# Kernel tuning notes

Measured on AMD Instinct MI355X. Metric: run time of the kernel, lower is better.

## Reference

```python
import jax, jax.numpy as jnp
import numpy as np

HEADS = 8
DIM_HEAD = 64
TOP_K = 1024
KMEANS_ITERS = 4  # the original KMeans class is external; we use Lloyd's algorithm, init = first TOP_K points


def chan_ln(x, g, b):
    # ChanLayerNorm3D: normalize over channel dim (axis=1), biased variance
    m = x.mean(axis=1, keepdims=True)
    v = x.var(axis=1, keepdims=True)
    return g.reshape(1, -1, 1, 1, 1) * (x - m) / (jnp.sqrt(v) + 1e-6) + b.reshape(1, -1, 1, 1, 1)


def kmeans_fit(x, k, iters):
    # x: [N, d] -> centroids [k, d]
    cent0 = x[:k]

    def step(_, cent):
        d2 = (x * x).sum(-1, keepdims=True) - 2.0 * (x @ cent.T) + (cent * cent).sum(-1)
        assign = jnp.argmin(d2, axis=-1)
        sums = jax.ops.segment_sum(x, assign, num_segments=k)
        cnt = jax.ops.segment_sum(jnp.ones((x.shape[0],), x.dtype), assign, num_segments=k)
        new = sums / jnp.maximum(cnt, 1.0)[:, None]
        return jnp.where(cnt[:, None] > 0, new, cent)  # keep old centroid for empty clusters

    return jax.lax.fori_loop(0, iters, step, cent0)


def select_best_idx(q, k, top_k):
    # q: [B, i, d], k: [B, j, d] -> indices [B, top_k] of keys farthest (L1) from their assigned q-centroid
    B, j, d = k.shape
    qf = q.reshape(-1, d)
    kf = k.reshape(-1, d)
    cent = kmeans_fit(qf, top_k, KMEANS_ITERS)
    d2 = (kf * kf).sum(-1, keepdims=True) - 2.0 * (kf @ cent.T) + (cent * cent).sum(-1)
    kc = jnp.argmin(d2, axis=-1)  # predict cluster of each key
    centers = cent[kc].reshape(B, j, d)
    dist = jnp.abs(centers - k).sum(-1)  # [B, j], L1 distance to assigned centroid
    return jnp.argsort(-dist, axis=1)[:, :top_k]


def dpca(query_source, context, w_q, w_kv, w_out, cn_g, cn_b, qn_g, qn_b, on_g, on_b, gamma):
    b, c, D, H, W = query_source.shape
    ctx = chan_ln(context, cn_g, cn_b)
    qs = chan_ln(query_source, qn_g, qn_b)
    # 1x1x1 convs == per-voxel channel matmuls
    kv = jnp.einsum('oc,bcdhw->bodhw', w_kv, ctx)
    k3, v3 = jnp.split(kv, 2, axis=1)
    q3 = jnp.einsum('oc,bcdhw->bodhw', w_q, qs)

    def fold_flat(t, norm):
        bb = t.shape[0]
        t = t.reshape(bb * HEADS, DIM_HEAD, *t.shape[2:])  # fold heads into batch
        if norm:  # F.normalize over channel dim, eps=1e-12
            t = t / jnp.maximum(jnp.linalg.norm(t, axis=1, keepdims=True), 1e-12)
        return t.reshape(bb * HEADS, DIM_HEAD, -1).transpose(0, 2, 1)  # [B, tokens, d]

    q = fold_flat(q3, True)
    k = fold_flat(k3, True)
    v = fold_flat(v3, False)

    idx = select_best_idx(jax.lax.stop_gradient(q), jax.lax.stop_gradient(k), TOP_K)
    k = jnp.take_along_axis(k, idx[:, :, None], axis=1)
    v = jnp.take_along_axis(v, idx[:, :, None], axis=1)

    attn = jax.nn.softmax(jnp.einsum('bid,bjd->bij', q, k), axis=-1)
    out = jnp.einsum('bij,bjd->bid', attn, v)
    out = out.reshape(b, HEADS, D, H, W, DIM_HEAD).transpose(0, 1, 5, 2, 3, 4)
    out = out.reshape(b, HEADS * DIM_HEAD, D, H, W)
    out = jnp.einsum('oc,bcdhw->bodhw', w_out, out)
    out = chan_ln(out, on_g, on_b)
    return gamma * out + query_source


def setup_inputs() -> dict:
    key = jax.random.key(0)
    ks = jax.random.split(key, 6)
    dim, inner, b = 256, HEADS * DIM_HEAD, 2
    query_source = jax.random.normal(ks[0], (b, dim, 16, 16, 16), jnp.float32)
    context = jax.random.normal(ks[1], (b, dim, 8, 16, 16), jnp.float32)
    s_in = 1.0 / np.sqrt(dim)
    return {
        'query_source': query_source,
        'context': context,
        'w_q': jax.random.normal(ks[2], (inner, dim), jnp.float32) * s_in,
        'w_kv': jax.random.normal(ks[3], (2 * inner, dim), jnp.float32) * s_in,
        'w_out': jax.random.normal(ks[4], (dim, inner), jnp.float32) * (1.0 / np.sqrt(inner)),
        'cn_g': jnp.ones((dim,), jnp.float32), 'cn_b': jnp.zeros((dim,), jnp.float32),
        'qn_g': jnp.ones((dim,), jnp.float32), 'qn_b': jnp.zeros((dim,), jnp.float32),
        'on_g': jnp.ones((dim,), jnp.float32), 'on_b': jnp.zeros((dim,), jnp.float32),
        'gamma': jnp.full((1,), 0.5, jnp.float32),  # torch inits to 0 (trivial output); 0.5 makes the test meaningful
    }


def reference(query_source, context, w_q, w_kv, w_out, cn_g, cn_b, qn_g, qn_b, on_g, on_b, gamma):
    return dpca(query_source, context, w_q, w_kv, w_out, cn_g, cn_b, qn_g, qn_b, on_g, on_b, gamma)
```

## Files before the change

### kernel.cpp

```cpp
#include <hip/hip_runtime.h>
#include <math.h>

#define BB 2
#define CDIM 256
#define NQ 4096
#define NK 2048
#define BH 16
#define TOPK 1024
#define NPQ (BH*NQ)
#define NPK (BH*NK)

typedef __attribute__((ext_vector_type(8))) short bfx8;
typedef __attribute__((ext_vector_type(8))) _Float16 hfx8;
typedef __attribute__((ext_vector_type(4))) float fx4;
typedef __attribute__((ext_vector_type(4))) unsigned short us4;

__device__ inline unsigned short f2bf(float x) {
  unsigned u = __float_as_uint(x);
  return (unsigned short)((u + 0x7fffu + ((u >> 16) & 1u)) >> 16);
}
__device__ inline unsigned short f2h_bits(float x) {
  _Float16 h = (_Float16)x;
  unsigned short u;
  __builtin_memcpy(&u, &h, 2);
  return u;
}
__device__ inline float h_bits2f(unsigned short u) {
  _Float16 h;
  __builtin_memcpy(&h, &u, 2);
  return (float)h;
}

__global__ __launch_bounds__(256) void chan_ln_tsplit_k(
    const float* __restrict__ x, const float* __restrict__ g,
    const float* __restrict__ bta, unsigned short* __restrict__ yh,
    unsigned short* __restrict__ yl, int C, int N) {
  __shared__ float tile[4][64][65];
  __shared__ float p1[4][64], p2[4][64];
  __shared__ float mArr[64], invArr[64];
  int t = threadIdx.x, lane = t & 63, wv = t >> 6;
  int n0 = blockIdx.x * 64, bi = blockIdx.y;
  const float* xb = x + (size_t)bi * C * N + n0 + lane;
  float s = 0.f, s2 = 0.f;
  for (int cl = 0; cl < 64; ++cl) {
    float v = xb[(size_t)(wv * 64 + cl) * N];
    tile[wv][cl][lane] = v;
    s += v;
    s2 += v * v;
  }
  p1[wv][lane] = s;
  p2[wv][lane] = s2;
  __syncthreads();
  if (t < 64) {
    float ts = p1[0][t] + p1[1][t] + p1[2][t] + p1[3][t];
    float ts2 = p2[0][t] + p2[1][t] + p2[2][t] + p2[3][t];
    float m = ts / C;
    float var = ts2 / C - m * m;
    mArr[t] = m;
    invArr[t] = 1.f / (sqrtf(fmaxf(var, 0.f)) + 1e-6f);
  }
  __syncthreads();
  int c = wv * 64 + lane;
  float gc = g[c], bc = bta[c];
  unsigned short* ohb = yh + ((size_t)bi * N + n0) * C + c;
  unsigned short* olb = yl + ((size_t)bi * N + n0) * C + c;
  for (int pl = 0; pl < 64; ++pl) {
    float v = tile[wv][lane][pl];
    float ln = gc * (v - mArr[pl]) * invArr[pl] + bc;
    unsigned short hb = f2h_bits(ln);
    ohb[(size_t)pl * C] = hb;
    olb[(size_t)pl * C] = f2h_bits((ln - h_bits2f(hb)) * 2048.f);
  }
}

__global__ __launch_bounds__(256) void gemm_mfma_k(
    const float* __restrict__ W, const unsigned short* __restrict__ Xh,
    const unsigned short* __restrict__ Xl, float* __restrict__ Y,
    int O, int C, int N) {
  int t = threadIdx.x, lane = t & 63, wv = t >> 6;
  int lq = lane & 15, lg = lane >> 4;
  int n0 = blockIdx.x * 64, o0 = blockIdx.y * 64 + wv * 16;
  int b = blockIdx.z;
  const unsigned short* xbh = Xh + ((size_t)b * N + n0) * C;
  const unsigned short* xbl = Xl + ((size_t)b * N + n0) * C;
  const float* wr = W + (size_t)(o0 + lq) * C;
  fx4 ahi[4], alo[4];
  for (int nt = 0; nt < 4; ++nt) {
    ahi[nt] = (fx4){0.f, 0.f, 0.f, 0.f};
    alo[nt] = (fx4){0.f, 0.f, 0.f, 0.f};
  }
  for (int k0 = 0; k0 < C; k0 += 32) {
    float4 w0 = *(const float4*)(wr + k0 + lg * 8);
    float4 w1 = *(const float4*)(wr + k0 + lg * 8 + 4);
    float wv8[8] = {w0.x, w0.y, w0.z, w0.w, w1.x, w1.y, w1.z, w1.w};
    hfx8 ah, al;
#pragma unroll
    for (int i = 0; i < 8; ++i) {
      _Float16 h = (_Float16)wv8[i];
      ah[i] = h;
      al[i] = (_Float16)((wv8[i] - (float)h) * 2048.f);
    }
#pragma unroll
    for (int nt = 0; nt < 4; ++nt) {
      const unsigned short* bph = xbh + (size_t)(nt * 16 + lq) * C + k0 + lg * 8;
      const unsigned short* bpl = xbl + (size_t)(nt * 16 + lq) * C + k0 + lg * 8;
      hfx8 bh = *(const hfx8*)bph;
      hfx8 bl = *(const hfx8*)bpl;
      ahi[nt] = __builtin_amdgcn_mfma_f32_16x16x32_f16(ah, bh, ahi[nt], 0, 0, 0);
      alo[nt] = __builtin_amdgcn_mfma_f32_16x16x32_f16(al, bh, alo[nt], 0, 0, 0);
      alo[nt] = __builtin_amdgcn_mfma_f32_16x16x32_f16(ah, bl, alo[nt], 0, 0, 0);
    }
  }
  float* yb = Y + ((size_t)b * O + o0) * N + n0;
#pragma unroll
  for (int nt = 0; nt < 4; ++nt)
#pragma unroll
    for (int r = 0; r < 4; ++r)
      yb[(size_t)(lg * 4 + r) * N + nt * 16 + lq] = ahi[nt][r] + alo[nt][r] * (1.f / 2048.f);
}

template <int PATH>
__global__ __launch_bounds__(256) void gemmfold_k(
    const float* __restrict__ W, const unsigned short* __restrict__ Xh,
    const unsigned short* __restrict__ Xl, float* __restrict__ fq,
    unsigned short* __restrict__ sh, unsigned short* __restrict__ sl,
    unsigned short* __restrict__ b16, float* __restrict__ fv,
    int C, int N) {
  __shared__ float ftile[64][65];
  __shared__ float part[4][64];
  __shared__ float invArr[64];
  int t = threadIdx.x, lane = t & 63, wv = t >> 6;
  int lq = lane & 15, lg = lane >> 4;
  int n0 = blockIdx.x * 64, o0 = blockIdx.y * 64 + wv * 16;
  int b = blockIdx.z;
  bool isV = (PATH == 1) && (blockIdx.y >= 8);
  int h = (PATH == 1) ? (blockIdx.y & 7) : blockIdx.y;
  const unsigned short* xbh = Xh + ((size_t)b * N + n0) * C;
  const unsigned short* xbl = Xl + ((size_t)b * N + n0) * C;
  const float* wr = W + (size_t)(o0 + lq) * C;
  fx4 ahi[4], alo[4];
  for (int nt = 0; nt < 4; ++nt) {
    ahi[nt] = (fx4){0.f, 0.f, 0.f, 0.f};
    alo[nt] = (fx4){0.f, 0.f, 0.f, 0.f};
  }
  for (int k0 = 0; k0 < C; k0 += 32) {
    float4 w0 = *(const float4*)(wr + k0 + lg * 8);
    float4 w1 = *(const float4*)(wr + k0 + lg * 8 + 4);
    float wv8[8] = {w0.x, w0.y, w0.z, w0.w, w1.x, w1.y, w1.z, w1.w};
    hfx8 ah, al;
#pragma unroll
    for (int i = 0; i < 8; ++i) {
      _Float16 hh = (_Float16)wv8[i];
      ah[i] = hh;
      al[i] = (_Float16)((wv8[i] - (float)hh) * 2048.f);
    }
#pragma unroll
    for (int nt = 0; nt < 4; ++nt) {
      const unsigned short* bph = xbh + (size_t)(nt * 16 + lq) * C + k0 + lg * 8;
      const unsigned short* bpl = xbl + (size_t)(nt * 16 + lq) * C + k0 + lg * 8;
      hfx8 bh = *(const hfx8*)bph;
      hfx8 bl = *(const hfx8*)bpl;
      ahi[nt] = __builtin_amdgcn_mfma_f32_16x16x32_f16(ah, bh, ahi[nt], 0, 0, 0);
      alo[nt] = __builtin_amdgcn_mfma_f32_16x16x32_f16(al, bh, alo[nt], 0, 0, 0);
      alo[nt] = __builtin_amdgcn_mfma_f32_16x16x32_f16(ah, bl, alo[nt], 0, 0, 0);
    }
  }
  float val[4][4];
#pragma unroll
  for (int nt = 0; nt < 4; ++nt)
#pragma unroll
    for (int r = 0; r < 4; ++r)
      val[nt][r] = ahi[nt][r] + alo[nt][r] * (1.f / 2048.f);
  if (!isV) {
#pragma unroll
    for (int nt = 0; nt < 4; ++nt) {
      float ss = val[nt][0] * val[nt][0] + val[nt][1] * val[nt][1] +
                 val[nt][2] * val[nt][2] + val[nt][3] * val[nt][3];
      ss += __shfl_xor(ss, 16);
      ss += __shfl_xor(ss, 32);
      if (lg == 0) part[wv][nt * 16 + lq] = ss;
    }
    __syncthreads();
    if (t < 64) {
      float tot = part[0][t] + part[1][t] + part[2][t] + part[3][t];
      invArr[t] = 1.f / fmaxf(sqrtf(tot), 1e-12f);
    }
    __syncthreads();
#pragma unroll
    for (int nt = 0; nt < 4; ++nt) {
      float iv = invArr[nt * 16 + lq];
#pragma unroll
      for (int r = 0; r < 4; ++r) val[nt][r] *= iv;
    }
    __syncthreads();
  }
#pragma unroll
  for (int nt = 0; nt < 4; ++nt)
#pragma unroll
    for (int r = 0; r < 4; ++r)
      ftile[nt * 16 + lq][wv * 16 + lg * 4 + r] = val[nt][r];
  __syncthreads();
  size_t rowb = (size_t)(b * 8 + h) * N + n0;
  for (int r2 = 0; r2 < 16; ++r2) {
    int n = r2 * 4 + wv;
    float v = ftile[n][lane];
    size_t idx = (rowb + n) * 64 + lane;
    if (PATH == 1 && isV) {
      fv[idx] = v;
    } else {
      fq[idx] = v;
      unsigned short hb = f2h_bits(v);
      sh[idx] = hb;
      sl[idx] = f2h_bits((v - h_bits2f(hb)) * 2048.f);
      if (PATH == 0) b16[idx] = f2bf(v);
    }
  }
}

__global__ void centprep_k(const float* __restrict__ cent, float* __restrict__ csq,
                           unsigned short* __restrict__ cb2h, unsigned short* __restrict__ cb2l) {
  int j = blockIdx.x, lane = threadIdx.x;
  float c = cent[j * 64 + lane];
  float s = c * c;
  for (int off = 32; off; off >>= 1) s += __shfl_xor(s, off);
  if (lane == 0) csq[j] = s;
  float m2 = -2.f * c;
  unsigned short h = f2h_bits(m2);
  cb2h[j * 64 + lane] = h;
  cb2l[j * 64 + lane] = f2h_bits((m2 - h_bits2f(h)) * 2048.f);
}

template <int DUO>
__global__ __launch_bounds__(256) void assign_mfma_k(
    const unsigned short* __restrict__ xh, const unsigned short* __restrict__ xl,
    const unsigned short* __restrict__ cb2h, const unsigned short* __restrict__ cb2l,
    const float* __restrict__ csq, int* __restrict__ aout) {
  __shared__ __align__(16) unsigned short clds[2][2][1024];
  int t = threadIdx.x, lane = t & 63, wv = t >> 6;
  int lq = lane & 15, lg = lane >> 4;
  int p0 = blockIdx.x * (DUO ? 128 : 64) + wv * (DUO ? 32 : 16);
  const unsigned short* xbA = xh + (size_t)(p0 + lq) * 64;
  const unsigned short* xlA = xl + (size_t)(p0 + lq) * 64;
  hfx8 ba0 = *(const hfx8*)(xbA + lg * 8);
  hfx8 ba1 = *(const hfx8*)(xbA + 32 + lg * 8);
  hfx8 la0 = *(const hfx8*)(xlA + lg * 8);
  hfx8 la1 = *(const hfx8*)(xlA + 32 + lg * 8);
  hfx8 bb0, bb1, lb0, lb1;
  if (DUO) {
    const unsigned short* xbB = xh + (size_t)(p0 + 16 + lq) * 64;
    const unsigned short* xlB = xl + (size_t)(p0 + 16 + lq) * 64;
    bb0 = *(const hfx8*)(xbB + lg * 8);
    bb1 = *(const hfx8*)(xbB + 32 + lg * 8);
    lb0 = *(const hfx8*)(xlB + lg * 8);
    lb1 = *(const hfx8*)(xlB + 32 + lg * 8);
  }

  int part = t >> 7;
  int abyte = (t & 127) * 16;
  int wbyte = abyte ^ (((abyte >> 7) & 7) << 4);
  const unsigned short* gsrc = (part ? cb2l : cb2h) + (abyte >> 1);
  int rowoff = lq * 128;
  int x0 = (lg * 16) ^ ((lq & 7) << 4);
  int x1 = (64 + lg * 16) ^ ((lq & 7) << 4);

  float bestA = 3.4e38f, bestB = 3.4e38f;
  int jA = 0, jB = 0;

  uint4 r0 = *(const uint4*)(gsrc);
  *(uint4*)((char*)&clds[0][part][0] + wbyte) = r0;

  for (int s = 0; s < 64; ++s) {
    int cur = s & 1;
    __syncthreads();
    uint4 rn;
    if (s < 63) rn = *(const uint4*)(gsrc + (size_t)(s + 1) * 1024);
    __builtin_amdgcn_sched_barrier(0);
    const char* ph = (const char*)&clds[cur][0][0];
    const char* pl = (const char*)&clds[cur][1][0];
    hfx8 ah0 = *(const hfx8*)(ph + rowoff + x0);
    hfx8 ah1 = *(const hfx8*)(ph + rowoff + x1);
    hfx8 al0 = *(const hfx8*)(pl + rowoff + x0);
    hfx8 al1 = *(const hfx8*)(pl + rowoff + x1);
    fx4 cq = *(const fx4*)(csq + s * 16 + lg * 4);
    {
      fx4 chi = cq;
      chi = __builtin_amdgcn_mfma_f32_16x16x32_f16(ah0, ba0, chi, 0, 0, 0);
      chi = __builtin_amdgcn_mfma_f32_16x16x32_f16(ah1, ba1, chi, 0, 0, 0);
      fx4 clo = (fx4){0.f, 0.f, 0.f, 0.f};
      clo = __builtin_amdgcn_mfma_f32_16x16x32_f16(ah0, la0, clo, 0, 0, 0);
      clo = __builtin_amdgcn_mfma_f32_16x16x32_f16(ah1, la1, clo, 0, 0, 0);
      clo = __builtin_amdgcn_mfma_f32_16x16x32_f16(al0, ba0, clo, 0, 0, 0);
      clo = __builtin_amdgcn_mfma_f32_16x16x32_f16(al1, ba1, clo, 0, 0, 0);
#pragma unroll
      for (int r_ = 0; r_ < 4; ++r_) {
        int j_ = s * 16 + lg * 4 + r_;
        float d2_ = chi[r_] + clo[r_] * (1.f / 2048.f);
        if (d2_ < bestA) { bestA = d2_; jA = j_; }
      }
    }
    if (DUO) {
      fx4 chi = cq;
      chi = __builtin_amdgcn_mfma_f32_16x16x32_f16(ah0, bb0, chi, 0, 0, 0);
      chi = __builtin_amdgcn_mfma_f32_16x16x32_f16(ah1, bb1, chi, 0, 0, 0);
      fx4 clo = (fx4){0.f, 0.f, 0.f, 0.f};
      clo = __builtin_amdgcn_mfma_f32_16x16x32_f16(ah0, lb0, clo, 0, 0, 0);
      clo = __builtin_amdgcn_mfma_f32_16x16x32_f16(ah1, lb1, clo, 0, 0, 0);
      clo = __builtin_amdgcn_mfma_f32_16x16x32_f16(al0, bb0, clo, 0, 0, 0);
      clo = __builtin_amdgcn_mfma_f32_16x16x32_f16(al1, bb1, clo, 0, 0, 0);
#pragma unroll
      for (int r_ = 0; r_ < 4; ++r_) {
        int j_ = s * 16 + lg * 4 + r_;
        float d2_ = chi[r_] + clo[r_] * (1.f / 2048.f);
        if (d2_ < bestB) { bestB = d2_; jB = j_; }
      }
    }
    __builtin_amdgcn_sched_barrier(0);
    if (s < 63) *(uint4*)((char*)&clds[cur ^ 1][part][0] + wbyte) = rn;
  }

  {
    float o = __shfl_xor(bestA, 16);
    int oj = __shfl_xor(jA, 16);
    if (o < bestA || (o == bestA && oj < jA)) { bestA = o; jA = oj; }
    o = __shfl_xor(bestA, 32);
    oj = __shfl_xor(jA, 32);
    if (o < bestA || (o == bestA && oj < jA)) { bestA = o; jA = oj; }
  }
  if (DUO) {
    float o = __shfl_xor(bestB, 16);
    int oj = __shfl_xor(jB, 16);
    if (o < bestB || (o == bestB && oj < jB)) { bestB = o; jB = oj; }
    o = __shfl_xor(bestB, 32);
    oj = __shfl_xor(jB, 32);
    if (o < bestB || (o == bestB && oj < jB)) { bestB = o; jB = oj; }
  }
  if (lg == 0) {
    aout[p0 + lq] = jA;
    if (DUO) aout[p0 + 16 + lq] = jB;
  }
}

__global__ void dist_k(const float* __restrict__ x, const float* __restrict__ cent,
                       const int* __restrict__ asg, float* __restrict__ dout) {
  int t = threadIdx.x, lane = t & 63, wv = t >> 6;
  int p = blockIdx.x * 4 + wv;
  int a = asg[p];
  float v = fabsf(cent[(size_t)a * 64 + lane] - x[(size_t)p * 64 + lane]);
  for (int off = 32; off; off >>= 1) v += __shfl_xor(v, off);
  if (lane == 0) dout[p] = v;
}

__global__ void segsum_k(const float* __restrict__ x, const int* __restrict__ asg,
                         float* __restrict__ sums, float* __restrict__ cnt) {
  int t = threadIdx.x, lane = t & 63, wv = t >> 6;
  int p = blockIdx.x * 4 + wv;
  int a = asg[p];
  float v = x[(size_t)p * 64 + lane];
  atomicAdd(&sums[a * 64 + lane], v);
  if (lane == 0) atomicAdd(&cnt[a], 1.0f);
}

__global__ __launch_bounds__(256) void centup_prep_k(
    float* __restrict__ cent, float* __restrict__ sums, float* __restrict__ cnt,
    float* __restrict__ csq, unsigned short* __restrict__ cb2h,
    unsigned short* __restrict__ cb2l) {
  int i = blockIdx.x * 256 + threadIdx.x;
  int j = i >> 6, lane = threadIdx.x & 63;
  float c = cnt[j];
  float oldc = cent[i];
  float newc = (c > 0.f) ? sums[i] / fmaxf(c, 1.f) : oldc;
  cent[i] = newc;
  float s = newc * newc;
  for (int off = 32; off; off >>= 1) s += __shfl_xor(s, off);
  if (lane == 0) csq[j] = s;
  float m2 = -2.f * newc;
  unsigned short h = f2h_bits(m2);
  cb2h[i] = h;
  cb2l[i] = f2h_bits((m2 - h_bits2f(h)) * 2048.f);
  sums[i] = 0.f;
  if (lane == 0) cnt[j] = 0.f;
}

__global__ __launch_bounds__(1024) void topk_k(const float* __restrict__ dist,
                                               int* __restrict__ sel) {
  __shared__ unsigned long long keys[2048];
  int bh = blockIdx.x, t = threadIdx.x;
  for (int i = t; i < 2048; i += 1024) {
    float d = dist[bh * 2048 + i];
    unsigned int db = __float_as_uint(d);
    keys[i] = ((unsigned long long)db << 32) | (unsigned int)(2047 - i);
  }
  __syncthreads();
  for (int k = 2; k <= 2048; k <<= 1) {
    for (int j = k >> 1; j > 0; j >>= 1) {
      for (int i = t; i < 2048; i += 1024) {
        int ixj = i ^ j;
        if (ixj > i) {
          unsigned long long a = keys[i], b = keys[ixj];
          bool up = ((i & k) == 0);
          bool sw = up ? (a < b) : (a > b);
          if (sw) { keys[i] = b; keys[ixj] = a; }
        }
      }
      __syncthreads();
    }
  }
  if (t < 1024) sel[bh * 1024 + t] = 2047 - (int)(keys[t] & 0xffffffffu);
}

__global__ void gatherb_k(const float* __restrict__ kbuf, const float* __restrict__ vbuf,
                          const int* __restrict__ sel, unsigned short* __restrict__ kh,
                          unsigned short* __restrict__ vT) {
  __shared__ unsigned short tile[64][66];
  int t = threadIdx.x, lane = t & 63, wv = t >> 6;
  int bh = blockIdx.y, i0 = blockIdx.x * 64;
  for (int r = 0; r < 16; ++r) {
    int i = r * 4 + wv;
    int src = sel[bh * 1024 + i0 + i];
    float kvv = kbuf[((size_t)bh * 2048 + src) * 64 + lane];
    kh[((size_t)bh * 1024 + i0 + i) * 64 + lane] = f2bf(kvv);
    float vv = vbuf[((size_t)bh * 2048 + src) * 64 + lane];
    tile[i][lane] = f2bf(vv);
  }
  __syncthreads();
  for (int r = 0; r < 16; ++r) {
    int d = r * 4 + wv;
    vT[((size_t)bh * 64 + d) * 1024 + i0 + lane] = tile[lane][d];
  }
}

__global__ __launch_bounds__(256) void attn_mfma_k(
    const unsigned short* __restrict__ qh, const unsigned short* __restrict__ kh,
    const unsigned short* __restrict__ vT,
    unsigned short* __restrict__ oh, unsigned short* __restrict__ ol) {
  __shared__ __align__(16) unsigned short kvlds[2][2][4096];
  __shared__ unsigned short plds[4][16][72];
  int t = threadIdx.x, lane = t & 63, wv = t >> 6;
  int lq = lane & 15, lg = lane >> 4;
  int bh = blockIdx.y;
  int q0 = blockIdx.x * 64 + wv * 16;
  const unsigned short* qbase = qh + ((size_t)bh * 4096 + q0 + lq) * 64;
  bfx8 qf0 = *(const bfx8*)(qbase + lg * 8);
  bfx8 qf1 = *(const bfx8*)(qbase + 32 + lg * 8);
  fx4 acc[4];
  for (int nt = 0; nt < 4; ++nt) acc[nt] = (fx4){0.f, 0.f, 0.f, 0.f};
  float lsum = 0.f;
  const unsigned short* kbase = kh + (size_t)bh * 1024 * 64;
  const unsigned short* vbase = vT + (size_t)bh * 64 * 1024;

  int srow = t >> 2;
  int scolb = (t & 3) * 32;
  const char* gK = (const char*)kbase + (size_t)srow * 128 + scolb;
  const char* gV = (const char*)vbase + (size_t)srow * 2048 + scolb;
  int sw_w = (srow & 7) << 4;
  int wb0 = srow * 128 + (scolb ^ sw_w);
  int wb1 = srow * 128 + ((scolb + 16) ^ sw_w);

  {
    uint4 k0 = *(const uint4*)(gK);
    uint4 k1 = *(const uint4*)(gK + 16);
    uint4 v0 = *(const uint4*)(gV);
    uint4 v1 = *(const uint4*)(gV + 16);
    *(uint4*)((char*)&kvlds[0][0][0] + wb0) = k0;
    *(uint4*)((char*)&kvlds[0][0][0] + wb1) = k1;
    *(uint4*)((char*)&kvlds[0][1][0] + wb0) = v0;
    *(uint4*)((char*)&kvlds[0][1][0] + wb1) = v1;
  }

  int swr = (lq & 7) << 4;
  int rc0 = (lg * 16) ^ swr;
  int rc1 = (64 + lg * 16) ^ swr;

  for (int s = 0; s < 16; ++s) {
    int cur = s & 1;
    __syncthreads();
    uint4 nk0, nk1, nv0, nv1;
    if (s < 15) {
      const char* gKn = gK + (size_t)(s + 1) * 8192;
      const char* gVn = gV + (size_t)(s + 1) * 128;
      nk0 = *(const uint4*)(gKn);
      nk1 = *(const uint4*)(gKn + 16);
      nv0 = *(const uint4*)(gVn);
      nv1 = *(const uint4*)(gVn + 16);
    }
    __builtin_amdgcn_sched_barrier(0);
    const char* Kb = (const char*)&kvlds[cur][0][0];
    const char* Vb = (const char*)&kvlds[cur][1][0];
    fx4 sS[4];
#pragma unroll
    for (int mt = 0; mt < 4; ++mt) {
      int rowb = (mt * 16 + lq) * 128;
      bfx8 a0 = *(const bfx8*)(Kb + rowb + rc0);
      bfx8 a1 = *(const bfx8*)(Kb + rowb + rc1);
      fx4 c = (fx4){0.f, 0.f, 0.f, 0.f};
      c = __builtin_amdgcn_mfma_f32_16x16x32_bf16(a0, qf0, c, 0, 0, 0);
      c = __builtin_amdgcn_mfma_f32_16x16x32_bf16(a1, qf1, c, 0, 0, 0);
      sS[mt] = c;
    }
#pragma unroll
    for (int mt = 0; mt < 4; ++mt) {
      float p0 = __expf(sS[mt].x), p1 = __expf(sS[mt].y);
      float p2 = __expf(sS[mt].z), p3 = __expf(sS[mt].w);
      lsum += (p0 + p1) + (p2 + p3);
      us4 pk = {f2bf(p0), f2bf(p1), f2bf(p2), f2bf(p3)};
      *(us4*)&plds[wv][lq][mt * 16 + lg * 4] = pk;
    }
    bfx8 pa0 = *(const bfx8*)&plds[wv][lq][lg * 8];
    bfx8 pa1 = *(const bfx8*)&plds[wv][lq][32 + lg * 8];
#pragma unroll
    for (int nt = 0; nt < 4; ++nt) {
      int rowb = (nt * 16 + lq) * 128;
      bfx8 b0 = *(const bfx8*)(Vb + rowb + rc0);
      bfx8 b1 = *(const bfx8*)(Vb + rowb + rc1);
      acc[nt] = __builtin_amdgcn_mfma_f32_16x16x32_bf16(pa0, b0, acc[nt], 0, 0, 0);
      acc[nt] = __builtin_amdgcn_mfma_f32_16x16x32_bf16(pa1, b1, acc[nt], 0, 0, 0);
    }
    __builtin_amdgcn_sched_barrier(0);
    if (s < 15) {
      char* dK = (char*)&kvlds[cur ^ 1][0][0];
      char* dV = (char*)&kvlds[cur ^ 1][1][0];
      *(uint4*)(dK + wb0) = nk0;
      *(uint4*)(dK + wb1) = nk1;
      *(uint4*)(dV + wb0) = nv0;
      *(uint4*)(dV + wb1) = nv1;
    }
  }
  lsum += __shfl_xor(lsum, 16);
  lsum += __shfl_xor(lsum, 32);
  int bi = bh >> 3, hd = bh & 7;
  for (int r = 0; r < 4; ++r) {
    float inv = 1.f / __shfl(lsum, lg * 4 + r);
    size_t rowb = ((size_t)bi * 4096 + q0 + lg * 4 + r) * 512 + hd * 64;
    for (int nt = 0; nt < 4; ++nt) {
      float val = acc[nt][r] * inv;
      unsigned short hb = f2h_bits(val);
      oh[rowb + nt * 16 + lq] = hb;
      ol[rowb + nt * 16 + lq] = f2h_bits((val - h_bits2f(hb)) * 2048.f);
    }
  }
}

__global__ __launch_bounds__(256) void final_k(
    const float* __restrict__ y, const float* __restrict__ g,
    const float* __restrict__ bta, const float* __restrict__ gamma,
    const float* __restrict__ qs, float* __restrict__ out) {
  __shared__ float p1[4][64], p2[4][64];
  __shared__ float mArr[64], invArr[64];
  int t = threadIdx.x, lane = t & 63, wv = t >> 6;
  int n0 = blockIdx.x * 64, bi = blockIdx.y;
  const float* yb = y + (size_t)bi * CDIM * NQ + n0 + lane;
  float s = 0.f, s2 = 0.f;
  for (int cl = 0; cl < 64; ++cl) {
    float v = yb[(size_t)(wv * 64 + cl) * NQ];
    s += v;
    s2 += v * v;
  }
  p1[wv][lane] = s;
  p2[wv][lane] = s2;
  __syncthreads();
  if (t < 64) {
    float ts = p1[0][t] + p1[1][t] + p1[2][t] + p1[3][t];
    float ts2 = p2[0][t] + p2[1][t] + p2[2][t] + p2[3][t];
    float m = ts / CDIM;
    float var = ts2 / CDIM - m * m;
    mArr[t] = m;
    invArr[t] = 1.f / (sqrtf(fmaxf(var, 0.f)) + 1e-6f);
  }
  __syncthreads();
  float gm = gamma[0];
  float m = mArr[lane], inv = invArr[lane];
  const float* qb = qs + (size_t)bi * CDIM * NQ + n0 + lane;
  float* ob = out + (size_t)bi * CDIM * NQ + n0 + lane;
  for (int cl = 0; cl < 64; ++cl) {
    int c = wv * 64 + cl;
    float v = yb[(size_t)c * NQ];
    float ln = g[c] * (v - m) * inv + bta[c];
    ob[(size_t)c * NQ] = gm * ln + qb[(size_t)c * NQ];
  }
}

extern "C" void kernel_launch(void* const* d_in, const int* in_sizes, int n_in,
                              void* d_out, int out_size, void* d_ws, size_t ws_size,
                              hipStream_t stream) {
  const float* qsrc = (const float*)d_in[0];
  const float* ctx = (const float*)d_in[1];
  const float* w_q = (const float*)d_in[2];
  const float* w_kv = (const float*)d_in[3];
  const float* w_out = (const float*)d_in[4];
  const float* cn_g = (const float*)d_in[5];
  const float* cn_b = (const float*)d_in[6];
  const float* qn_g = (const float*)d_in[7];
  const float* qn_b = (const float*)d_in[8];
  const float* on_g = (const float*)d_in[9];
  const float* on_b = (const float*)d_in[10];
  const float* gamma = (const float*)d_in[11];

  if (ws_size < (size_t)22267904 * 4) return;
  float* ws = (float*)d_ws;
  float* r_ctx = ws;
  float* r_kv = r_ctx + 1048576;
  float* r_qs = r_kv + 4194304;
  float* r_q3 = r_qs + 2097152;
  float* qbuf = r_q3 + 4194304;
  float* kbuf = qbuf + 4194304;
  float* vbuf = kbuf + 2097152;
  float* cent = vbuf + 2097152;
  float* csq = cent + 65536;
  float* sums = csq + 1024;
  float* cnt = sums + 65536;
  int* asg = (int*)(cnt + 1024);
  float* dist = (float*)(asg + 65536);
  int* sel = (int*)(dist + 32768);
  float* kgreg = (float*)(sel + 16384);

  unsigned short* ctxth = (unsigned short*)r_ctx;
  unsigned short* ctxtl = ctxth + (size_t)BB * NK * CDIM;
  unsigned short* qsth = (unsigned short*)r_qs;
  unsigned short* qstl = qsth + (size_t)BB * NQ * CDIM;
  unsigned short* qh = (unsigned short*)kgreg;
  unsigned short* kh = (unsigned short*)r_ctx;
  unsigned short* vT = kh + 1048576;
  unsigned short* qbh = (unsigned short*)r_q3;
  unsigned short* qbl = qbh + (size_t)NPQ * 64;
  unsigned short* kbh = (unsigned short*)r_kv;
  unsigned short* kbl = kbh + (size_t)NPK * 64;
  unsigned short* cb2h = (unsigned short*)r_qs;
  unsigned short* cb2l = cb2h + 65536;
  unsigned short* attnth = (unsigned short*)r_kv;
  unsigned short* attntl = attnth + (size_t)BB * NQ * 512;
  float* ybuf = r_qs;

  chan_ln_tsplit_k<<<dim3(NK / 64, BB), 256, 0, stream>>>(ctx, cn_g, cn_b, ctxth, ctxtl, CDIM, NK);
  chan_ln_tsplit_k<<<dim3(NQ / 64, BB), 256, 0, stream>>>(qsrc, qn_g, qn_b, qsth, qstl, CDIM, NQ);
  gemmfold_k<1><<<dim3(NK / 64, 16, BB), 256, 0, stream>>>(
      w_kv, ctxth, ctxtl, kbuf, kbh, kbl, nullptr, vbuf, CDIM, NK);
  gemmfold_k<0><<<dim3(NQ / 64, 8, BB), 256, 0, stream>>>(
      w_q, qsth, qstl, qbuf, qbh, qbl, qh, nullptr, CDIM, NQ);
  hipMemcpyAsync(cent, qbuf, 65536 * sizeof(float), hipMemcpyDeviceToDevice, stream);
  centprep_k<<<1024, 64, 0, stream>>>(cent, csq, cb2h, cb2l);
  hipMemsetAsync(sums, 0, (65536 + 1024) * sizeof(float), stream);
  for (int it = 0; it < 4; ++it) {
    assign_mfma_k<1><<<NPQ / 128, 256, 0, stream>>>(qbh, qbl, cb2h, cb2l, csq, asg);
    segsum_k<<<NPQ / 4, 256, 0, stream>>>(qbuf, asg, sums, cnt);
    centup_prep_k<<<65536 / 256, 256, 0, stream>>>(cent, sums, cnt, csq, cb2h, cb2l);
  }
  assign_mfma_k<0><<<NPK / 64, 256, 0, stream>>>(kbh, kbl, cb2h, cb2l, csq, asg);
  dist_k<<<NPK / 4, 256, 0, stream>>>(kbuf, cent, asg, dist);
  topk_k<<<BH, 1024, 0, stream>>>(dist, sel);
  gatherb_k<<<dim3(TOPK / 64, BH), 256, 0, stream>>>(kbuf, vbuf, sel, kh, vT);
  attn_mfma_k<<<dim3(NQ / 64, BH), 256, 0, stream>>>(qh, kh, vT, attnth, attntl);
  gemm_mfma_k<<<dim3(NQ / 64, 256 / 64, BB), 256, 0, stream>>>(w_out, attnth, attntl, ybuf, 256, 512, NQ);
  final_k<<<dim3(NQ / 64, BB), 256, 0, stream>>>(ybuf, on_g, on_b, gamma, qsrc, (float*)d_out);
}
```

Baseline: 588.4 us.

## Stage activation tiles through double-buffered swizzled LDS in gemmfold kernel

The projection GEMM with fold and normalize now copies the fp16 hi/lo activation tiles into a double-buffered LDS area with an XOR swizzle, and prefetches the next K-slice of activations and weights into registers while the MFMAs run on the current slice. Before this, each wave read B operands straight from global memory with strided per-row loads, and the four waves re-read the same tile. The change adds LDS pressure and a barrier per K-step, which may reduce occupancy. This is one kernel among several in the pipeline.

After: 537.1 us. 1.1x faster.

```diff
diff --git a/kernel.cpp b/kernel.cpp
--- a/kernel.cpp
+++ b/kernel.cpp
@@ -126,6 +126,7 @@
     unsigned short* __restrict__ sh, unsigned short* __restrict__ sl,
     unsigned short* __restrict__ b16, float* __restrict__ fv,
     int C, int N) {
+  __shared__ __align__(16) unsigned short xlds[2][64][64];
   __shared__ float ftile[64][65];
   __shared__ float part[4][64];
   __shared__ float invArr[64];
@@ -138,15 +139,47 @@
   const unsigned short* xbh = Xh + ((size_t)b * N + n0) * C;
   const unsigned short* xbl = Xl + ((size_t)b * N + n0) * C;
   const float* wr = W + (size_t)(o0 + lq) * C;
+
+  int a = t * 16;
+  int srow = a >> 6;
+  int schunk = (a >> 4) & 3;
+  const unsigned short* gsh = xbh + (size_t)srow * C + schunk * 8;
+  const unsigned short* gsl = xbl + (size_t)srow * C + schunk * 8;
+  int swz = (srow & 7) << 4;
+  int wbh = srow * 128 + ((schunk * 16) ^ swz);
+  int wbl = srow * 128 + ((64 + schunk * 16) ^ swz);
+  int rswz = (lq & 7) << 4;
+  int xh0 = (lg * 16) ^ rswz;
+  int xl0 = (64 + lg * 16) ^ rswz;
+
   fx4 ahi[4], alo[4];
   for (int nt = 0; nt < 4; ++nt) {
     ahi[nt] = (fx4){0.f, 0.f, 0.f, 0.f};
     alo[nt] = (fx4){0.f, 0.f, 0.f, 0.f};
   }
-  for (int k0 = 0; k0 < C; k0 += 32) {
-    float4 w0 = *(const float4*)(wr + k0 + lg * 8);
-    float4 w1 = *(const float4*)(wr + k0 + lg * 8 + 4);
-    float wv8[8] = {w0.x, w0.y, w0.z, w0.w, w1.x, w1.y, w1.z, w1.w};
+
+  {
+    uint4 h0 = *(const uint4*)(gsh);
+    uint4 l0 = *(const uint4*)(gsl);
+    *(uint4*)((char*)&xlds[0][0][0] + wbh) = h0;
+    *(uint4*)((char*)&xlds[0][0][0] + wbl) = l0;
+  }
+  float4 w0c = *(const float4*)(wr + lg * 8);
+  float4 w1c = *(const float4*)(wr + lg * 8 + 4);
+
+  for (int s = 0; s < 8; ++s) {
+    int cur = s & 1;
+    __syncthreads();
+    uint4 nh, nl;
+    float4 nw0, nw1;
+    if (s < 7) {
+      nh = *(const uint4*)(gsh + (s + 1) * 32);
+      nl = *(const uint4*)(gsl + (s + 1) * 32);
+      nw0 = *(const float4*)(wr + (s + 1) * 32 + lg * 8);
+      nw1 = *(const float4*)(wr + (s + 1) * 32 + lg * 8 + 4);
+    }
+    __builtin_amdgcn_sched_barrier(0);
+    float wv8[8] = {w0c.x, w0c.y, w0c.z, w0c.w, w1c.x, w1c.y, w1c.z, w1c.w};
     hfx8 ah, al;
 #pragma unroll
     for (int i = 0; i < 8; ++i) {
@@ -154,23 +187,32 @@
       ah[i] = hh;
       al[i] = (_Float16)((wv8[i] - (float)hh) * 2048.f);
     }
+    const char* Xb = (const char*)&xlds[cur][0][0];
 #pragma unroll
     for (int nt = 0; nt < 4; ++nt) {
-      const unsigned short* bph = xbh + (size_t)(nt * 16 + lq) * C + k0 + lg * 8;
-      const unsigned short* bpl = xbl + (size_t)(nt * 16 + lq) * C + k0 + lg * 8;
-      hfx8 bh = *(const hfx8*)bph;
-      hfx8 bl = *(const hfx8*)bpl;
+      int rb = (nt * 16 + lq) * 128;
+      hfx8 bh = *(const hfx8*)(Xb + rb + xh0);
+      hfx8 bl = *(const hfx8*)(Xb + rb + xl0);
       ahi[nt] = __builtin_amdgcn_mfma_f32_16x16x32_f16(ah, bh, ahi[nt], 0, 0, 0);
       alo[nt] = __builtin_amdgcn_mfma_f32_16x16x32_f16(al, bh, alo[nt], 0, 0, 0);
       alo[nt] = __builtin_amdgcn_mfma_f32_16x16x32_f16(ah, bl, alo[nt], 0, 0, 0);
     }
-  }
+    __builtin_amdgcn_sched_barrier(0);
+    if (s < 7) {
+      *(uint4*)((char*)&xlds[cur ^ 1][0][0] + wbh) = nh;
+      *(uint4*)((char*)&xlds[cur ^ 1][0][0] + wbl) = nl;
+      w0c = nw0;
+      w1c = nw1;
+    }
+  }
+
   float val[4][4];
 #pragma unroll
   for (int nt = 0; nt < 4; ++nt)
 #pragma unroll
     for (int r = 0; r < 4; ++r)
       val[nt][r] = ahi[nt][r] + alo[nt][r] * (1.f / 2048.f);
+  __syncthreads();
   if (!isV) {
 #pragma unroll
     for (int nt = 0; nt < 4; ++nt) {
```
